# Kernel tuning notes

Hardware: AMD Instinct MI355X
Metric: run time of the kernel (lower is better)

Reference implementation:

```python
import jax, jax.numpy as jnp
import numpy as np

N = 200000   # num_nodes
D = 64       # embedding_dims
B = 4096     # batch of target nodes (batched per-edge processing)
K = 128      # padded in-neighbor count per target
W = 20       # window_size (history deque length)
H = 128      # hidden_size


def setup_inputs() -> dict:
    key = jax.random.key(0)
    ks = jax.random.split(key, 14)
    return {
        "adj_time": jax.random.uniform(ks[0], (N,), jnp.float32),          # last-seen times in [0,1)
        "gc": jax.random.uniform(ks[1], (N,), jnp.float32),                 # per-node centrality scalar (dict_gc)
        "cur_time": jnp.ones((1,), jnp.float32),                            # current event time (>= all stored times)
        "neigh_mask": jnp.ones((B, K), jnp.float32),                        # 1 = valid neighbor slot
        "hist_feat": jax.random.normal(ks[2], (B, W, 2 * D), jnp.float32),  # feature_dict[...]['feature'] deque
        "hist_time": jax.random.uniform(ks[3], (B, W), jnp.float32),        # feature_dict[...]['time'] deque
        "t2v_w": jax.random.normal(ks[4], (D,), jnp.float32),               # Time2Vec('cos') weights
        "t2v_b": jax.random.normal(ks[5], (D,), jnp.float32),
        "node_w": jax.random.normal(ks[6], (D,), jnp.float32),              # linear_node: Linear(1, D)
        "node_b": jax.random.normal(ks[7], (D,), jnp.float32),
        "att_w": jax.random.normal(ks[8], (2 * D,), jnp.float32),           # Attention: score = cat(a,b) @ w + b
        "att_b": jax.random.normal(ks[9], (1,), jnp.float32),
        "weight": jax.random.normal(ks[10], (H, 4 * D), jnp.float32) * 0.05,
        "targets": jax.random.randint(ks[11], (B,), 0, N),
        "neigh_idx": jax.random.randint(ks[12], (B, K), 0, N),
    }


def reference(adj_time, gc, cur_time, neigh_mask, hist_feat, hist_time,
              t2v_w, t2v_b, node_w, node_b, att_w, att_b, weight,
              targets, neigh_idx):
    t = cur_time[0]

    def node_encoding(idx):
        # Time2Vec('cos'): first channel linear, rest cos(w*dt+b)
        dt = jnp.abs(t - adj_time[idx])[..., None]            # [..., 1]
        phase = t2v_w * dt + t2v_b                            # [..., D]
        tv = jnp.concatenate([phase[..., :1], jnp.cos(phase[..., 1:])], axis=-1)
        feat = jax.nn.relu(tv + gc[idx][..., None] * node_w + node_b)
        # F.normalize (L2 over feature dim)
        return feat / jnp.maximum(jnp.linalg.norm(feat, axis=-1, keepdims=True), 1e-12)

    tgt_feat = node_encoding(targets)       # [B, D]
    ngh_feat = node_encoding(neigh_idx)     # [B, K, D]

    # Decayer(2, 'log'): time_score = 1 / (2 * log(e + dt))
    time_score = 1.0 / (2.0 * jnp.log(jnp.e + (t - adj_time[neigh_idx])))   # [B, K]
    # Attention score between target and each neighbor encoding
    att = (tgt_feat @ att_w[:D])[:, None] \
        + jnp.einsum("bkd,d->bk", ngh_feat, att_w[D:]) + att_b[0]           # [B, K]
    score = jax.nn.leaky_relu(time_score + att, 0.01) * neigh_mask          # [B, K]
    neigh_agg = jnp.einsum("bk,bkd->bd", score, ngh_feat)                   # [B, D]

    combined = jnp.concatenate([tgt_feat, neigh_agg], axis=-1)              # [B, 2D]

    # History aggregation with Decayer(2, 'rev'): w = 1 / (2 * (1 + dt))
    hist_w = 1.0 / (2.0 * (1.0 + (t - hist_time)))                          # [B, W]
    hist_agg = jnp.einsum("bw,bwd->bd", hist_w, hist_feat)                  # [B, 2D]

    feat4 = jnp.concatenate([hist_agg, combined], axis=-1)                  # [B, 4D]
    return jax.nn.relu(feat4 @ weight.T)                                    # [B, H]
```

## Files before the change

kernel.cpp:

```cpp
#include <hip/hip_runtime.h>
#include <math.h>

#define NN 200000
#define DD 64
#define BB 4096
#define KK 128
#define WW 20
#define HH 128

__device__ __forceinline__ float fast_rcp(float x) { return __builtin_amdgcn_rcpf(x); }
__device__ __forceinline__ float fast_rsq(float x) { return __builtin_amdgcn_rsqf(x); }

__global__ __launch_bounds__(256) void k1_encode(
    const float* __restrict__ adj_time, const float* __restrict__ gc,
    const float* __restrict__ cur_time, const float* __restrict__ neigh_mask,
    const float* __restrict__ hist_feat, const float* __restrict__ hist_time,
    const float* __restrict__ t2v_w, const float* __restrict__ t2v_b,
    const float* __restrict__ node_w, const float* __restrict__ node_b,
    const float* __restrict__ att_w, const float* __restrict__ att_b,
    const int* __restrict__ targets, const int* __restrict__ neigh_idx,
    float* __restrict__ feat4)
{
    const int b    = blockIdx.x;
    const int tid  = threadIdx.x;
    const int lane = tid & 63;
    const int wid  = tid >> 6;

    __shared__ float4 p4[64];
    __shared__ float  aw2s[64];
    __shared__ float  hws[WW];
    __shared__ float  hpart[128];
    __shared__ float  fnL[128 * 65];
    __shared__ float  s2h[128];
    __shared__ float  sdh[128];
    __shared__ float  wk[128];
    __shared__ float  aggp[4][64];
    __shared__ float  stL;

    const float t = cur_time[0];

    if (tid < 64) {
        p4[tid]   = make_float4(t2v_w[tid], t2v_b[tid], node_w[tid], node_b[tid]);
        aw2s[tid] = att_w[64 + tid];
    }
    if (tid < WW) {
        hws[tid] = fast_rcp(2.0f * (1.0f + (t - hist_time[b * WW + tid])));
    }
    __syncthreads();

    float hsum;
    {
        int half = tid >> 7;
        int d    = tid & 127;
        const float* hf = hist_feat + (size_t)b * WW * 128 + d;
        float s = 0.f;
#pragma unroll
        for (int w = 0; w < 10; ++w) {
            int ww = half * 10 + w;
            s = fmaf(hws[ww], hf[ww * 128], s);
        }
        if (half) hpart[d] = s;
        hsum = s;
    }

    if (wid == 0) {
        int   tg  = targets[b];
        float dtT = fabsf(t - adj_time[tg]);
        float gT  = gc[tg];
        float4 p  = p4[lane];
        float ph  = fmaf(p.x, dtT, p.y);
        float tv  = (lane == 0) ? ph : __cosf(ph);
        float f   = fmaxf(tv + fmaf(gT, p.z, p.w), 0.f);
        float ss  = f * f;
#pragma unroll
        for (int off = 32; off; off >>= 1) ss += __shfl_xor(ss, off, 64);
        float invn = fast_rsq(fmaxf(ss, 1e-24f));
        float tfn  = f * invn;
        float sdt  = tfn * att_w[lane];
#pragma unroll
        for (int off = 32; off; off >>= 1) sdt += __shfl_xor(sdt, off, 64);
        if (lane == 0) stL = sdt;
        feat4[b * 256 + 128 + lane] = tfn;
    }

    const int   k    = tid & 127;
    const int   half = tid >> 7;
    const int   idx  = neigh_idx[b * KK + k];
    const float at   = adj_time[idx];
    const float g    = gc[idx];
    const float dtN  = fabsf(t - at);

    __syncthreads();

    if (!half) {
        int d = tid & 127;
        feat4[b * 256 + d] = hsum + hpart[d];
    }

    float s2 = 0.f, sd = 0.f;
    {
        float* fnRow = fnL + k * 65 + half * 32;
#pragma unroll
        for (int dd = 0; dd < 32; ++dd) {
            int    d  = half * 32 + dd;
            float4 p  = p4[d];
            float  ph = fmaf(p.x, dtN, p.y);
            float  cv = __cosf(ph);
            float  tv = (d == 0) ? ph : cv;
            float  f  = fmaxf(tv + fmaf(g, p.z, p.w), 0.f);
            fnRow[dd] = f;
            s2 = fmaf(f, f, s2);
            sd = fmaf(f, aw2s[d], sd);
        }
    }
    if (half) { s2h[k] = s2; sdh[k] = sd; }
    __syncthreads();

    if (!half) {
        s2 += s2h[k];
        sd += sdh[k];
        float invn = fast_rsq(fmaxf(s2, 1e-24f));
        float ts   = fast_rcp(2.0f * __logf(2.71828182845904523536f + (t - at)));
        float m    = neigh_mask[b * KK + k];
        float sc   = ts + stL + sd * invn + att_b[0];
        sc = (sc > 0.f) ? sc : 0.01f * sc;
        wk[k] = sc * m * invn;
    }
    __syncthreads();

    float acc = 0.f;
    {
        const int k0 = wid * 32;
#pragma unroll
        for (int j = 0; j < 32; ++j) {
            acc = fmaf(wk[k0 + j], fnL[(k0 + j) * 65 + lane], acc);
        }
    }
    aggp[wid][lane] = acc;
    __syncthreads();
    if (tid < 64) {
        feat4[b * 256 + 192 + tid] =
            aggp[0][tid] + aggp[1][tid] + aggp[2][tid] + aggp[3][tid];
    }
}

__global__ __launch_bounds__(256) void k2_gemm(
    const float* __restrict__ feat4, const float* __restrict__ weight,
    float* __restrict__ out)
{
    const int b0  = blockIdx.x * 8;
    const int tid = threadIdx.x;

    __shared__ float tile[8 * 256];
    __shared__ float wl[128 * 33];

    {
        const float4* src = (const float4*)(feat4 + (size_t)b0 * 256);
        float4* dst = (float4*)tile;
        dst[tid]       = src[tid];
        dst[tid + 256] = src[tid + 256];
    }

    const int h = tid & 127;
    const int g = tid >> 7;
    const float* tb = tile + (g * 4) * 256;

    float acc0 = 0.f, acc1 = 0.f, acc2 = 0.f, acc3 = 0.f;

    for (int c = 0; c < 8; ++c) {
        __syncthreads();
#pragma unroll
        for (int i = 0; i < 16; ++i) {
            int l  = i * 256 + tid;
            int hh = l >> 5;
            int jj = l & 31;
            wl[hh * 33 + jj] = weight[hh * 256 + c * 32 + jj];
        }
        __syncthreads();

#pragma unroll
        for (int jj = 0; jj < 32; jj += 4) {
            float w0 = wl[h * 33 + jj + 0];
            float w1 = wl[h * 33 + jj + 1];
            float w2 = wl[h * 33 + jj + 2];
            float w3 = wl[h * 33 + jj + 3];
            float4 f0 = *(const float4*)(tb + 0 * 256 + c * 32 + jj);
            float4 f1 = *(const float4*)(tb + 1 * 256 + c * 32 + jj);
            float4 f2 = *(const float4*)(tb + 2 * 256 + c * 32 + jj);
            float4 f3 = *(const float4*)(tb + 3 * 256 + c * 32 + jj);
            acc0 += w0 * f0.x + w1 * f0.y + w2 * f0.z + w3 * f0.w;
            acc1 += w0 * f1.x + w1 * f1.y + w2 * f1.z + w3 * f1.w;
            acc2 += w0 * f2.x + w1 * f2.y + w2 * f2.z + w3 * f2.w;
            acc3 += w0 * f3.x + w1 * f3.y + w2 * f3.z + w3 * f3.w;
        }
    }

    out[(size_t)(b0 + g * 4 + 0) * 128 + h] = fmaxf(acc0, 0.f);
    out[(size_t)(b0 + g * 4 + 1) * 128 + h] = fmaxf(acc1, 0.f);
    out[(size_t)(b0 + g * 4 + 2) * 128 + h] = fmaxf(acc2, 0.f);
    out[(size_t)(b0 + g * 4 + 3) * 128 + h] = fmaxf(acc3, 0.f);
}

extern "C" void kernel_launch(void* const* d_in, const int* in_sizes, int n_in,
                              void* d_out, int out_size, void* d_ws, size_t ws_size,
                              hipStream_t stream) {
    const float* adj_time  = (const float*)d_in[0];
    const float* gc        = (const float*)d_in[1];
    const float* cur_time  = (const float*)d_in[2];
    const float* neigh_mask= (const float*)d_in[3];
    const float* hist_feat = (const float*)d_in[4];
    const float* hist_time = (const float*)d_in[5];
    const float* t2v_w     = (const float*)d_in[6];
    const float* t2v_b     = (const float*)d_in[7];
    const float* node_w    = (const float*)d_in[8];
    const float* node_b    = (const float*)d_in[9];
    const float* att_w     = (const float*)d_in[10];
    const float* att_b     = (const float*)d_in[11];
    const float* weight    = (const float*)d_in[12];
    const int*   targets   = (const int*)d_in[13];
    const int*   neigh_idx = (const int*)d_in[14];

    float* out   = (float*)d_out;
    float* feat4 = (float*)d_ws;

    k1_encode<<<BB, 256, 0, stream>>>(adj_time, gc, cur_time, neigh_mask,
                                      hist_feat, hist_time, t2v_w, t2v_b,
                                      node_w, node_b, att_w, att_b,
                                      targets, neigh_idx, feat4);

    k2_gemm<<<BB / 8, 256, 0, stream>>>(feat4, weight, out);
}
```

Before: 140.9 us.

## Recompute neighbor encodings instead of staging 33KB feature tile in LDS

```diff
diff --git a/kernel.cpp b/kernel.cpp
--- a/kernel.cpp
+++ b/kernel.cpp
@@ -25,52 +25,39 @@
     const int tid  = threadIdx.x;
     const int lane = tid & 63;
     const int wid  = tid >> 6;
-
-    __shared__ float4 p4[64];
-    __shared__ float  aw2s[64];
+    const int k    = tid & 127;
+    const int half = tid >> 7;
+
     __shared__ float  hws[WW];
     __shared__ float  hpart[128];
-    __shared__ float  fnL[128 * 65];
-    __shared__ float  s2h[128];
-    __shared__ float  sdh[128];
-    __shared__ float  wk[128];
+    __shared__ float4 dtg[128];
+    __shared__ float2 sp[2][128];
     __shared__ float  aggp[4][64];
     __shared__ float  stL;
 
     const float t = cur_time[0];
 
-    if (tid < 64) {
-        p4[tid]   = make_float4(t2v_w[tid], t2v_b[tid], node_w[tid], node_b[tid]);
-        aw2s[tid] = att_w[64 + tid];
-    }
-    if (tid < WW) {
-        hws[tid] = fast_rcp(2.0f * (1.0f + (t - hist_time[b * WW + tid])));
-    }
-    __syncthreads();
-
-    float hsum;
-    {
-        int half = tid >> 7;
-        int d    = tid & 127;
-        const float* hf = hist_feat + (size_t)b * WW * 128 + d;
-        float s = 0.f;
-#pragma unroll
-        for (int w = 0; w < 10; ++w) {
-            int ww = half * 10 + w;
-            s = fmaf(hws[ww], hf[ww * 128], s);
-        }
-        if (half) hpart[d] = s;
-        hsum = s;
-    }
-
-    if (wid == 0) {
+    float ts_k = 0.f, m_k = 0.f;
+    if (tid < 128) {
+        int   idx = neigh_idx[b * KK + k];
+        m_k       = neigh_mask[b * KK + k];
+        float at  = adj_time[idx];
+        float g   = gc[idx];
+        float dt  = fabsf(t - at);
+        dtg[k]    = make_float4(dt, g, 0.f, 0.f);
+        ts_k      = fast_rcp(2.0f * __logf(2.71828182845904523536f + (t - at)));
+    } else if (wid == 2) {
+        if (lane < WW)
+            hws[lane] = fast_rcp(2.0f * (1.0f + (t - hist_time[b * WW + lane])));
+    } else {
         int   tg  = targets[b];
         float dtT = fabsf(t - adj_time[tg]);
         float gT  = gc[tg];
-        float4 p  = p4[lane];
-        float ph  = fmaf(p.x, dtT, p.y);
+        float pw  = t2v_w[lane], pb = t2v_b[lane];
+        float nw  = node_w[lane], nb2 = node_b[lane];
+        float ph  = fmaf(pw, dtT, pb);
         float tv  = (lane == 0) ? ph : __cosf(ph);
-        float f   = fmaxf(tv + fmaf(gT, p.z, p.w), 0.f);
+        float f   = fmaxf(tv + fmaf(gT, nw, nb2), 0.f);
         float ss  = f * f;
 #pragma unroll
         for (int off = 32; off; off >>= 1) ss += __shfl_xor(ss, off, 64);
@@ -82,62 +69,73 @@
         if (lane == 0) stL = sdt;
         feat4[b * 256 + 128 + lane] = tfn;
     }
-
-    const int   k    = tid & 127;
-    const int   half = tid >> 7;
-    const int   idx  = neigh_idx[b * KK + k];
-    const float at   = adj_time[idx];
-    const float g    = gc[idx];
-    const float dtN  = fabsf(t - at);
+    __syncthreads();
+
+    float hv[10];
+    {
+        const float* hf = hist_feat + (size_t)b * WW * 128 + (tid & 127);
+#pragma unroll
+        for (int w = 0; w < 10; ++w) hv[w] = hf[(half * 10 + w) * 128];
+    }
+
+    {
+        const int du0 = __builtin_amdgcn_readfirstlane(half * 32);
+        float4 dg = dtg[k];
+        float  dt = dg.x, g = dg.y;
+        float  s2 = 0.f, sd = 0.f;
+#pragma unroll
+        for (int dd = 0; dd < 32; ++dd) {
+            int   d   = du0 + dd;
+            float pw  = t2v_w[d], pb = t2v_b[d];
+            float nw  = node_w[d], nb2 = node_b[d];
+            float a2  = att_w[64 + d];
+            float ph  = fmaf(pw, dt, pb);
+            float cv  = __cosf(ph);
+            float tv  = (d == 0) ? ph : cv;
+            float f   = fmaxf(tv + fmaf(g, nw, nb2), 0.f);
+            s2 = fmaf(f, f, s2);
+            sd = fmaf(f, a2, sd);
+        }
+        sp[half][k] = make_float2(s2, sd);
+    }
+
+    float hsum = 0.f;
+#pragma unroll
+    for (int w = 0; w < 10; ++w) hsum = fmaf(hws[half * 10 + w], hv[w], hsum);
+    if (half) hpart[tid & 127] = hsum;
 
     __syncthreads();
 
     if (!half) {
-        int d = tid & 127;
-        feat4[b * 256 + d] = hsum + hpart[d];
-    }
-
-    float s2 = 0.f, sd = 0.f;
-    {
-        float* fnRow = fnL + k * 65 + half * 32;
-#pragma unroll
-        for (int dd = 0; dd < 32; ++dd) {
-            int    d  = half * 32 + dd;
-            float4 p  = p4[d];
-            float  ph = fmaf(p.x, dtN, p.y);
+        feat4[b * 256 + (tid & 127)] = hsum + hpart[tid & 127];
+        float2 a0 = sp[0][k], a1 = sp[1][k];
+        float  s2 = a0.x + a1.x;
+        float  sd = a0.y + a1.y;
+        float  invn = fast_rsq(fmaxf(s2, 1e-24f));
+        float  sc = ts_k + stL + sd * invn + att_b[0];
+        sc = (sc > 0.f) ? sc : 0.01f * sc;
+        dtg[k].z = sc * m_k * invn;
+    }
+    __syncthreads();
+
+    {
+        float pw  = t2v_w[lane], pb = t2v_b[lane];
+        float nw  = node_w[lane], nb2 = node_b[lane];
+        float acc = 0.f;
+        const int k0 = wid * 32;
+#pragma unroll 8
+        for (int j = 0; j < 32; ++j) {
+            float4 dg = dtg[k0 + j];
+            float  ph = fmaf(pw, dg.x, pb);
             float  cv = __cosf(ph);
-            float  tv = (d == 0) ? ph : cv;
-            float  f  = fmaxf(tv + fmaf(g, p.z, p.w), 0.f);
-            fnRow[dd] = f;
-            s2 = fmaf(f, f, s2);
-            sd = fmaf(f, aw2s[d], sd);
-        }
-    }
-    if (half) { s2h[k] = s2; sdh[k] = sd; }
-    __syncthreads();
-
-    if (!half) {
-        s2 += s2h[k];
-        sd += sdh[k];
-        float invn = fast_rsq(fmaxf(s2, 1e-24f));
-        float ts   = fast_rcp(2.0f * __logf(2.71828182845904523536f + (t - at)));
-        float m    = neigh_mask[b * KK + k];
-        float sc   = ts + stL + sd * invn + att_b[0];
-        sc = (sc > 0.f) ? sc : 0.01f * sc;
-        wk[k] = sc * m * invn;
-    }
-    __syncthreads();
-
-    float acc = 0.f;
-    {
-        const int k0 = wid * 32;
-#pragma unroll
-        for (int j = 0; j < 32; ++j) {
-            acc = fmaf(wk[k0 + j], fnL[(k0 + j) * 65 + lane], acc);
-        }
-    }
-    aggp[wid][lane] = acc;
-    __syncthreads();
+            float  tv = (lane == 0) ? ph : cv;
+            float  f  = fmaxf(tv + fmaf(dg.y, nw, nb2), 0.f);
+            acc = fmaf(dg.z, f, acc);
+        }
+        aggp[wid][lane] = acc;
+    }
+    __syncthreads();
+
     if (tid < 64) {
         feat4[b * 256 + 192 + tid] =
             aggp[0][tid] + aggp[1][tid] + aggp[2][tid] + aggp[3][tid];
```

Result: faster. 137.0 us (-2.8%).
